# Performance work log

Hardware: AMD Instinct MI355X
Metric: run time of the kernel (lower is better)

The kernel has to match this reference:

```python
import jax, jax.numpy as jnp
import numpy as np

N_NODES = 100000
N_EDGES = 1600000
IN_CH, HID = 4, 64


def setup_inputs() -> dict:
    key = jax.random.key(0)
    ks = jax.random.split(key, 10)
    x = jax.random.normal(ks[0], (N_NODES, IN_CH), dtype=jnp.float32)
    edge_index = jax.random.randint(ks[1], (2, N_EDGES), 0, N_NODES, dtype=jnp.int64)

    def lin(k, fin, fout):
        s = 1.0 / np.sqrt(fin)
        return jax.random.uniform(k, (fin, fout), jnp.float32, -s, s)

    return {
        "x": x,
        "edge_index": edge_index,
        "W1": lin(ks[2], IN_CH, HID), "b1": jnp.zeros((HID,), jnp.float32),
        "W2": lin(ks[3], HID, HID), "b2": jnp.zeros((HID,), jnp.float32),
        "lpW1": lin(ks[4], 2 * HID, HID), "lpb1": jnp.zeros((HID,), jnp.float32),
        "lpW2": lin(ks[5], HID, 1), "lpb2": jnp.zeros((1,), jnp.float32),
    }


def reference(x, edge_index, W1, b1, W2, b2, lpW1, lpb1, lpW2, lpb2):
    n = x.shape[0]
    src, dst = edge_index[0], edge_index[1]
    # GCN normalization with self-loops (PyG GCNConv defaults)
    loop = jnp.arange(n)
    s = jnp.concatenate([src, loop])  # [E+N]
    d = jnp.concatenate([dst, loop])
    deg = jax.ops.segment_sum(jnp.ones_like(s, dtype=x.dtype), d, num_segments=n)
    dinv = jnp.where(deg > 0, jax.lax.rsqrt(deg), 0.0)
    norm = dinv[s] * dinv[d]  # [E+N]

    def gcn_conv(h, W, b):
        hw = h @ W                               # [N, HID]
        msg = hw[s] * norm[:, None]              # gather + scale
        return jax.ops.segment_sum(msg, d, num_segments=n) + b

    h = jax.nn.relu(gcn_conv(x, W1, b1))
    h = jax.nn.relu(gcn_conv(h, W2, b2))  # node embeddings [N, HID]

    # edge scoring: gather-concat -> 2-layer MLP
    ef = jnp.concatenate([h[src], h[dst]], axis=1)  # [E, 2*HID]
    logits = (jax.nn.relu(ef @ lpW1 + lpb1) @ lpW2 + lpb2).squeeze(-1)  # [E]
    return logits
```

## Files before the change

### kernel.cpp

```cpp
#include <hip/hip_runtime.h>
#include <hip/hip_fp16.h>

#define NN 100000
#define NE 1600000
#define HH 64
#define BSH 9
#define NBUK 196

typedef unsigned long long u64;

__device__ __forceinline__ u64 epack(int s, int d, int e) {
    return (u64)(unsigned)s | ((u64)(unsigned)d << 17) | ((u64)(unsigned)e << 34);
}
__device__ __forceinline__ int esrc(u64 w) { return (int)(w & 0x1FFFF); }
__device__ __forceinline__ int edst(u64 w) { return (int)((w >> 17) & 0x1FFFF); }
__device__ __forceinline__ int eeid(u64 w) { return (int)(w >> 34); }


__global__ __launch_bounds__(1024) void k_bhist(const int* __restrict__ dst,
                                                int* __restrict__ bcnt) {
    __shared__ int cnt[NBUK];
    int tid = threadIdx.x;
    if (tid < NBUK) cnt[tid] = 0;
    __syncthreads();
    int e0 = blockIdx.x * 4096 + tid;
    #pragma unroll
    for (int i = 0; i < 4; ++i) {
        int e = e0 + i * 1024;
        if (e < NE) atomicAdd(&cnt[dst[e] >> BSH], 1);
    }
    __syncthreads();
    if (tid < NBUK && cnt[tid] > 0) atomicAdd(&bcnt[tid], cnt[tid]);
}


__global__ void k_bscan(const int* __restrict__ bcnt, int* __restrict__ bbase,
                        int* __restrict__ bcur) {
    __shared__ int sh[256];
    int tid = threadIdx.x;
    int v = (tid < NBUK) ? bcnt[tid] : 0;
    sh[tid] = v;
    __syncthreads();
    for (int off = 1; off < 256; off <<= 1) {
        int t = (tid >= off) ? sh[tid - off] : 0;
        __syncthreads();
        sh[tid] += t;
        __syncthreads();
    }
    if (tid < NBUK) {
        int ex = sh[tid] - v;
        bbase[tid] = ex;
        bcur[tid] = ex;
    }
    if (tid == 0) bbase[NBUK] = NE;
}


__global__ __launch_bounds__(1024) void k_partA(const int* __restrict__ src,
                                                const int* __restrict__ dst,
                                                int* __restrict__ bcur,
                                                u64* __restrict__ partA) {
    __shared__ int cnt[NBUK], off[NBUK], base[NBUK];
    int tid = threadIdx.x;
    if (tid < NBUK) { cnt[tid] = 0; off[tid] = 0; }
    __syncthreads();
    int e0 = blockIdx.x * 4096 + tid;
    int d0 = 0, d1 = 0, d2 = 0, d3 = 0;
    if (e0 < NE)            { d0 = dst[e0];            atomicAdd(&cnt[d0 >> BSH], 1); }
    if (e0 + 1024 < NE)     { d1 = dst[e0 + 1024];     atomicAdd(&cnt[d1 >> BSH], 1); }
    if (e0 + 2048 < NE)     { d2 = dst[e0 + 2048];     atomicAdd(&cnt[d2 >> BSH], 1); }
    if (e0 + 3072 < NE)     { d3 = dst[e0 + 3072];     atomicAdd(&cnt[d3 >> BSH], 1); }
    __syncthreads();
    if (tid < NBUK && cnt[tid] > 0) base[tid] = atomicAdd(&bcur[tid], cnt[tid]);
    __syncthreads();
    if (e0 < NE) {
        int b = d0 >> BSH; int o = atomicAdd(&off[b], 1);
        partA[base[b] + o] = epack(src[e0], d0, e0);
    }
    if (e0 + 1024 < NE) {
        int b = d1 >> BSH; int o = atomicAdd(&off[b], 1);
        partA[base[b] + o] = epack(src[e0 + 1024], d1, e0 + 1024);
    }
    if (e0 + 2048 < NE) {
        int b = d2 >> BSH; int o = atomicAdd(&off[b], 1);
        partA[base[b] + o] = epack(src[e0 + 2048], d2, e0 + 2048);
    }
    if (e0 + 3072 < NE) {
        int b = d3 >> BSH; int o = atomicAdd(&off[b], 1);
        partA[base[b] + o] = epack(src[e0 + 3072], d3, e0 + 3072);
    }
}


__global__ __launch_bounds__(1024) void k_partB2(const int* __restrict__ bbase,
                                                 const u64* __restrict__ partA,
                                                 u64* __restrict__ ecsr,
                                                 int* __restrict__ ptr,
                                                 float* __restrict__ dinv) {
    __shared__ int cnt[512], sc[512], cur[512];
    int b = blockIdx.x, tid = threadIdx.x;
    int nd0 = b << BSH;
    int nnode = NN - nd0; if (nnode > 512) nnode = 512;
    if (tid < 512) cnt[tid] = 0;
    __syncthreads();
    int pbeg = bbase[b], pend = bbase[b + 1];
    for (int p = pbeg + tid; p < pend; p += 1024)
        atomicAdd(&cnt[edst(partA[p]) - nd0], 1);
    __syncthreads();
    if (tid < 512) sc[tid] = cnt[tid];
    __syncthreads();
    for (int off = 1; off < 512; off <<= 1) {
        int t = (tid < 512 && tid >= off) ? sc[tid - off] : 0;
        __syncthreads();
        if (tid < 512) sc[tid] += t;
        __syncthreads();
    }
    if (tid < nnode) {
        int p = pbeg + sc[tid] - cnt[tid];
        ptr[nd0 + tid] = p;
        cur[tid] = p;
        dinv[nd0 + tid] = rsqrtf((float)(cnt[tid] + 1));
    }
    if (b == NBUK - 1 && tid == 0) ptr[NN] = NE;
    __syncthreads();
    for (int p = pbeg + tid; p < pend; p += 1024) {
        u64 t = partA[p];
        int pos = atomicAdd(&cur[edst(t) - nd0], 1);
        ecsr[pos] = t;
    }
}


__global__ void k_mm1(const float* __restrict__ x, const float* __restrict__ W1,
                      const float* __restrict__ dinv, __half* __restrict__ g) {
    __shared__ float w[4 * HH];
    w[threadIdx.x] = W1[threadIdx.x];
    __syncthreads();
    int idx = blockIdx.x * 256 + threadIdx.x;
    int i = idx >> 6, j = idx & 63;
    float4 xv = *reinterpret_cast<const float4*>(&x[i * 4]);
    float s = fmaf(xv.x, w[j],
              fmaf(xv.y, w[HH + j],
              fmaf(xv.z, w[2 * HH + j],
                   xv.w * w[3 * HH + j])));
    g[idx] = __float2half(s * dinv[i]);
}


__global__ void k_agg(const __half* __restrict__ g, const float* __restrict__ dinv,
                      const int* __restrict__ ptr, const u64* __restrict__ ecsr,
                      const float* __restrict__ bias, __half* __restrict__ h) {
    int node = blockIdx.x * 4 + (threadIdx.x >> 6);
    int lane = threadIdx.x & 63;
    if (node >= NN) return;
    float acc = __half2float(g[node * HH + lane]);
    int e0 = ptr[node], e1 = ptr[node + 1];
    int deg = e1 - e0;
    int lim = deg < 64 ? deg : 64;
    int c = (lane < deg) ? esrc(ecsr[e0 + lane]) : 0;
    int j = 0;
    for (; j + 16 <= lim; j += 16) {
        int s0 = __builtin_amdgcn_readlane(c, j);
        int s1 = __builtin_amdgcn_readlane(c, j + 1);
        int s2 = __builtin_amdgcn_readlane(c, j + 2);
        int s3 = __builtin_amdgcn_readlane(c, j + 3);
        int s4 = __builtin_amdgcn_readlane(c, j + 4);
        int s5 = __builtin_amdgcn_readlane(c, j + 5);
        int s6 = __builtin_amdgcn_readlane(c, j + 6);
        int s7 = __builtin_amdgcn_readlane(c, j + 7);
        int s8 = __builtin_amdgcn_readlane(c, j + 8);
        int s9 = __builtin_amdgcn_readlane(c, j + 9);
        int sa = __builtin_amdgcn_readlane(c, j + 10);
        int sb = __builtin_amdgcn_readlane(c, j + 11);
        int sc = __builtin_amdgcn_readlane(c, j + 12);
        int sd = __builtin_amdgcn_readlane(c, j + 13);
        int se = __builtin_amdgcn_readlane(c, j + 14);
        int sf = __builtin_amdgcn_readlane(c, j + 15);
        __half a0 = g[s0 * HH + lane];
        __half a1 = g[s1 * HH + lane];
        __half a2 = g[s2 * HH + lane];
        __half a3 = g[s3 * HH + lane];
        __half a4 = g[s4 * HH + lane];
        __half a5 = g[s5 * HH + lane];
        __half a6 = g[s6 * HH + lane];
        __half a7 = g[s7 * HH + lane];
        __half a8 = g[s8 * HH + lane];
        __half a9 = g[s9 * HH + lane];
        __half aa = g[sa * HH + lane];
        __half ab = g[sb * HH + lane];
        __half ac = g[sc * HH + lane];
        __half ad = g[sd * HH + lane];
        __half ae = g[se * HH + lane];
        __half af = g[sf * HH + lane];
        acc += ((__half2float(a0) + __half2float(a1)) + (__half2float(a2) + __half2float(a3)))
             + ((__half2float(a4) + __half2float(a5)) + (__half2float(a6) + __half2float(a7)));
        acc += ((__half2float(a8) + __half2float(a9)) + (__half2float(aa) + __half2float(ab)))
             + ((__half2float(ac) + __half2float(ad)) + (__half2float(ae) + __half2float(af)));
    }
    for (; j + 4 <= lim; j += 4) {
        int s0 = __builtin_amdgcn_readlane(c, j);
        int s1 = __builtin_amdgcn_readlane(c, j + 1);
        int s2 = __builtin_amdgcn_readlane(c, j + 2);
        int s3 = __builtin_amdgcn_readlane(c, j + 3);
        __half a0 = g[s0 * HH + lane];
        __half a1 = g[s1 * HH + lane];
        __half a2 = g[s2 * HH + lane];
        __half a3 = g[s3 * HH + lane];
        acc += (__half2float(a0) + __half2float(a1)) + (__half2float(a2) + __half2float(a3));
    }
    for (; j < lim; ++j) {
        int s = __builtin_amdgcn_readlane(c, j);
        acc += __half2float(g[s * HH + lane]);
    }
    for (int e = e0 + 64; e < e1; ++e) {
        acc += __half2float(g[esrc(ecsr[e]) * HH + lane]);
    }
    h[node * HH + lane] = __float2half(fmaxf(fmaf(acc, dinv[node], bias[lane]), 0.f));
}


__global__ void k_mm2(const __half* __restrict__ in, const float* __restrict__ W,
                      const float* __restrict__ dinv, __half* __restrict__ out) {
    __shared__ float w[HH * HH];
    __shared__ float row[16][HH + 4];
    for (int t = threadIdx.x; t < HH * HH; t += 256) w[t] = W[t];
    {
        int flat = threadIdx.x * 4;
        int r = flat >> 6, c = flat & 63;
        int node = blockIdx.x * 16 + r;
        uint2 v = *reinterpret_cast<const uint2*>(&in[node * HH + c]);
        float2 lo = __half22float2(*reinterpret_cast<__half2*>(&v.x));
        float2 hi = __half22float2(*reinterpret_cast<__half2*>(&v.y));
        row[r][c] = lo.x; row[r][c + 1] = lo.y; row[r][c + 2] = hi.x; row[r][c + 3] = hi.y;
    }
    __syncthreads();
    int r = threadIdx.x >> 4;
    int cg = (threadIdx.x & 15) * 4;
    int node = blockIdx.x * 16 + r;
    float4 acc = {0.f, 0.f, 0.f, 0.f};
    #pragma unroll
    for (int k = 0; k < HH; ++k) {
        float rk = row[r][k];
        float4 wv = *reinterpret_cast<const float4*>(&w[k * HH + cg]);
        acc.x = fmaf(rk, wv.x, acc.x);
        acc.y = fmaf(rk, wv.y, acc.y);
        acc.z = fmaf(rk, wv.z, acc.z);
        acc.w = fmaf(rk, wv.w, acc.w);
    }
    float dv = dinv[node];
    __half2 h01 = __floats2half2_rn(acc.x * dv, acc.y * dv);
    __half2 h23 = __floats2half2_rn(acc.z * dv, acc.w * dv);
    *reinterpret_cast<__half2*>(&out[node * HH + cg])     = h01;
    *reinterpret_cast<__half2*>(&out[node * HH + cg + 2]) = h23;
}


__global__ void k_proj(const __half* __restrict__ h, const float* __restrict__ lpW1,
                       const float* __restrict__ lpb1,
                       __half* __restrict__ A, __half* __restrict__ B) {
    __shared__ float w[128 * HH];
    __shared__ float row[16][HH + 4];
    for (int t = threadIdx.x; t < 128 * HH; t += 256) w[t] = lpW1[t];
    {
        int flat = threadIdx.x * 4;
        int r = flat >> 6, c = flat & 63;
        int node = blockIdx.x * 16 + r;
        uint2 v = *reinterpret_cast<const uint2*>(&h[node * HH + c]);
        float2 lo = __half22float2(*reinterpret_cast<__half2*>(&v.x));
        float2 hi = __half22float2(*reinterpret_cast<__half2*>(&v.y));
        row[r][c] = lo.x; row[r][c + 1] = lo.y; row[r][c + 2] = hi.x; row[r][c + 3] = hi.y;
    }
    __syncthreads();
    int r = threadIdx.x >> 4;
    int cg = (threadIdx.x & 15) * 4;
    int node = blockIdx.x * 16 + r;
    float4 acca = *reinterpret_cast<const float4*>(&lpb1[cg]);
    float4 accb = {0.f, 0.f, 0.f, 0.f};
    #pragma unroll
    for (int k = 0; k < HH; ++k) {
        float rk = row[r][k];
        float4 wa = *reinterpret_cast<const float4*>(&w[k * HH + cg]);
        float4 wb = *reinterpret_cast<const float4*>(&w[(HH + k) * HH + cg]);
        acca.x = fmaf(rk, wa.x, acca.x);
        acca.y = fmaf(rk, wa.y, acca.y);
        acca.z = fmaf(rk, wa.z, acca.z);
        acca.w = fmaf(rk, wa.w, acca.w);
        accb.x = fmaf(rk, wb.x, accb.x);
        accb.y = fmaf(rk, wb.y, accb.y);
        accb.z = fmaf(rk, wb.z, accb.z);
        accb.w = fmaf(rk, wb.w, accb.w);
    }
    __half2 a01 = __floats2half2_rn(acca.x, acca.y);
    __half2 a23 = __floats2half2_rn(acca.z, acca.w);
    __half2 b01 = __floats2half2_rn(accb.x, accb.y);
    __half2 b23 = __floats2half2_rn(accb.z, accb.w);
    *reinterpret_cast<__half2*>(&A[node * HH + cg])     = a01;
    *reinterpret_cast<__half2*>(&A[node * HH + cg + 2]) = a23;
    *reinterpret_cast<__half2*>(&B[node * HH + cg])     = b01;
    *reinterpret_cast<__half2*>(&B[node * HH + cg + 2]) = b23;
}


__device__ inline void acc8(float& acc, float4 av, float4 bv, const float* w8) {
    const __half2* ah = reinterpret_cast<const __half2*>(&av);
    const __half2* bh = reinterpret_cast<const __half2*>(&bv);
    #pragma unroll
    for (int i = 0; i < 4; ++i) {
        float2 a = __half22float2(ah[i]);
        float2 b = __half22float2(bh[i]);
        acc = fmaf(fmaxf(a.x + b.x, 0.f), w8[2 * i],     acc);
        acc = fmaf(fmaxf(a.y + b.y, 0.f), w8[2 * i + 1], acc);
    }
}

__global__ void k_edge(const u64* __restrict__ ecsr,
                       const __half* __restrict__ A, const __half* __restrict__ B,
                       const float* __restrict__ lpW2, const float* __restrict__ lpb2,
                       float* __restrict__ out) {
    __shared__ float w[HH];
    if (threadIdx.x < HH) w[threadIdx.x] = lpW2[threadIdx.x];
    __syncthreads();
    int lane = threadIdx.x & 63;
    int wv   = threadIdx.x >> 6;
    int sub  = lane & 3;
    int g    = lane >> 2;
    int base = (blockIdx.x * 4 + wv) * 32;
    u64 t0 = ecsr[base + g];
    u64 t1 = ecsr[base + 16 + g];
    const float4* pa0 = reinterpret_cast<const float4*>(&A[esrc(t0) * HH]) + sub * 2;
    const float4* pb0 = reinterpret_cast<const float4*>(&B[edst(t0) * HH]) + sub * 2;
    const float4* pa1 = reinterpret_cast<const float4*>(&A[esrc(t1) * HH]) + sub * 2;
    const float4* pb1 = reinterpret_cast<const float4*>(&B[edst(t1) * HH]) + sub * 2;
    float4 a00 = pa0[0], a01 = pa0[1];
    float4 b00 = pb0[0], b01 = pb0[1];
    float4 a10 = pa1[0], a11 = pa1[1];
    float4 b10 = pb1[0], b11 = pb1[1];
    const float* w16 = &w[sub * 16];
    float acc0 = 0.f, acc1 = 0.f;
    acc8(acc0, a00, b00, w16);
    acc8(acc0, a01, b01, w16 + 8);
    acc8(acc1, a10, b10, w16);
    acc8(acc1, a11, b11, w16 + 8);
    acc0 += __shfl_xor(acc0, 1);
    acc0 += __shfl_xor(acc0, 2);
    acc1 += __shfl_xor(acc1, 1);
    acc1 += __shfl_xor(acc1, 2);
    if (sub == 0) {
        float c0 = lpb2[0];
        out[eeid(t0)] = acc0 + c0;
        out[eeid(t1)] = acc1 + c0;
    }
}


extern "C" void kernel_launch(void* const* d_in, const int* in_sizes, int n_in,
                              void* d_out, int out_size, void* d_ws, size_t ws_size,
                              hipStream_t stream) {
    const float* x    = (const float*)d_in[0];
    const int*   ei   = (const int*)d_in[1];
    const float* W1   = (const float*)d_in[2];
    const float* b1   = (const float*)d_in[3];
    const float* W2   = (const float*)d_in[4];
    const float* b2   = (const float*)d_in[5];
    const float* lpW1 = (const float*)d_in[6];
    const float* lpb1 = (const float*)d_in[7];
    const float* lpW2 = (const float*)d_in[8];
    const float* lpb2 = (const float*)d_in[9];
    const int* src = ei;
    const int* dst = ei + NE;
    float* logits = (float*)d_out;

    char* ws = (char*)d_ws;
    size_t o = 0;
    auto take = [&](size_t bytes) { void* p = ws + o; o = (o + bytes + 255) & ~(size_t)255; return p; };
    float*  dinv   = (float*) take(NN * sizeof(float));
    int*    ptr    = (int*)   take((NN + 1) * sizeof(int));
    int*    bcnt   = (int*)   take(NBUK * sizeof(int));
    int*    bbase  = (int*)   take((NBUK + 1) * sizeof(int));
    int*    bcur   = (int*)   take(NBUK * sizeof(int));
    u64*    ecsr   = (u64*)   take((size_t)NE * sizeof(u64));
    char*   bufA   = (char*)  take((size_t)NE * sizeof(u64));
    __half* bufB   = (__half*)take((size_t)NN * HH * sizeof(__half));
    __half* bufC   = (__half*)take((size_t)NN * HH * sizeof(__half));
    u64*    partA  = (u64*)bufA;
    __half* g1h    = (__half*)bufA;
    __half* h2     = (__half*)bufA;
    __half* h1     = bufB;
    __half* Ah     = bufB;
    __half* g2h    = bufC;
    __half* Bh     = bufC;

    hipMemsetAsync(bcnt, 0, NBUK * sizeof(int), stream);
    k_bhist<<<(NE + 4095) / 4096, 1024, 0, stream>>>(dst, bcnt);
    k_bscan<<<1, 256, 0, stream>>>(bcnt, bbase, bcur);
    k_partA<<<(NE + 4095) / 4096, 1024, 0, stream>>>(src, dst, bcur, partA);
    k_partB2<<<NBUK, 1024, 0, stream>>>(bbase, partA, ecsr, ptr, dinv);

    k_mm1<<<(NN * HH) / 256, 256, 0, stream>>>(x, W1, dinv, g1h);
    k_agg<<<(NN + 3) / 4, 256, 0, stream>>>(g1h, dinv, ptr, ecsr, b1, h1);

    k_mm2<<<NN / 16, 256, 0, stream>>>(h1, W2, dinv, g2h);
    k_agg<<<(NN + 3) / 4, 256, 0, stream>>>(g2h, dinv, ptr, ecsr, b2, h2);

    k_proj<<<NN / 16, 256, 0, stream>>>(h2, lpW1, lpb1, Ah, Bh);

    k_edge<<<NE / 128, 256, 0, stream>>>(ecsr, Ah, Bh, lpW2, lpb2, logits);
}
```

Baseline: 267.9 us.

## Fuse first-layer matmul into CSR build and add compact 32-bit source index array

The x@W1 scaled by dinv computation moves into the k_partB2 CSR-building kernel, which drops the separate k_mm1 launch. k_partB2 also writes a separate 4-byte source-index array, so the two aggregation passes read 4 bytes per edge instead of 8. Workspace buffers are reassigned so that g1 no longer aliases partA while partA is still being read. In exchange, the 196 blocks of k_partB2 now do extra per-node work, and the extra scsr write adds 6.4MB of traffic.

```diff
diff --git a/kernel.cpp b/kernel.cpp
--- a/kernel.cpp
+++ b/kernel.cpp
@@ -95,10 +95,16 @@
 __global__ __launch_bounds__(1024) void k_partB2(const int* __restrict__ bbase,
                                                  const u64* __restrict__ partA,
                                                  u64* __restrict__ ecsr,
+                                                 int* __restrict__ scsr,
                                                  int* __restrict__ ptr,
-                                                 float* __restrict__ dinv) {
+                                                 float* __restrict__ dinv,
+                                                 const float* __restrict__ x,
+                                                 const float* __restrict__ W1,
+                                                 __half* __restrict__ g1) {
     __shared__ int cnt[512], sc[512], cur[512];
+    __shared__ float w1[4 * HH];
     int b = blockIdx.x, tid = threadIdx.x;
+    if (tid < 4 * HH) w1[tid] = W1[tid];
     int nd0 = b << BSH;
     int nnode = NN - nd0; if (nnode > 512) nnode = 512;
     if (tid < 512) cnt[tid] = 0;
@@ -127,28 +133,25 @@
         u64 t = partA[p];
         int pos = atomicAdd(&cur[edst(t) - nd0], 1);
         ecsr[pos] = t;
-    }
-}
-
-
-__global__ void k_mm1(const float* __restrict__ x, const float* __restrict__ W1,
-                      const float* __restrict__ dinv, __half* __restrict__ g) {
-    __shared__ float w[4 * HH];
-    w[threadIdx.x] = W1[threadIdx.x];
-    __syncthreads();
-    int idx = blockIdx.x * 256 + threadIdx.x;
-    int i = idx >> 6, j = idx & 63;
-    float4 xv = *reinterpret_cast<const float4*>(&x[i * 4]);
-    float s = fmaf(xv.x, w[j],
-              fmaf(xv.y, w[HH + j],
-              fmaf(xv.z, w[2 * HH + j],
-                   xv.w * w[3 * HH + j])));
-    g[idx] = __float2half(s * dinv[i]);
+        scsr[pos] = esrc(t);
+    }
+    int total = nnode * HH;
+    for (int i = tid; i < total; i += 1024) {
+        int ln = i >> 6, ch = i & 63;
+        int node = nd0 + ln;
+        float4 xv = *reinterpret_cast<const float4*>(&x[node * 4]);
+        float dv = rsqrtf((float)(cnt[ln] + 1));
+        float s = fmaf(xv.x, w1[ch],
+                  fmaf(xv.y, w1[HH + ch],
+                  fmaf(xv.z, w1[2 * HH + ch],
+                       xv.w * w1[3 * HH + ch])));
+        g1[node * HH + ch] = __float2half(s * dv);
+    }
 }
 
 
 __global__ void k_agg(const __half* __restrict__ g, const float* __restrict__ dinv,
-                      const int* __restrict__ ptr, const u64* __restrict__ ecsr,
+                      const int* __restrict__ ptr, const int* __restrict__ scsr,
                       const float* __restrict__ bias, __half* __restrict__ h) {
     int node = blockIdx.x * 4 + (threadIdx.x >> 6);
     int lane = threadIdx.x & 63;
@@ -157,7 +160,7 @@
     int e0 = ptr[node], e1 = ptr[node + 1];
     int deg = e1 - e0;
     int lim = deg < 64 ? deg : 64;
-    int c = (lane < deg) ? esrc(ecsr[e0 + lane]) : 0;
+    int c = (lane < deg) ? scsr[e0 + lane] : 0;
     int j = 0;
     for (; j + 16 <= lim; j += 16) {
         int s0 = __builtin_amdgcn_readlane(c, j);
@@ -213,7 +216,7 @@
         acc += __half2float(g[s * HH + lane]);
     }
     for (int e = e0 + 64; e < e1; ++e) {
-        acc += __half2float(g[esrc(ecsr[e]) * HH + lane]);
+        acc += __half2float(g[scsr[e] * HH + lane]);
     }
     h[node * HH + lane] = __float2half(fmaxf(fmaf(acc, dinv[node], bias[lane]), 0.f));
 }
@@ -379,28 +382,28 @@
     int*    bbase  = (int*)   take((NBUK + 1) * sizeof(int));
     int*    bcur   = (int*)   take(NBUK * sizeof(int));
     u64*    ecsr   = (u64*)   take((size_t)NE * sizeof(u64));
+    int*    scsr   = (int*)   take((size_t)NE * sizeof(int));
     char*   bufA   = (char*)  take((size_t)NE * sizeof(u64));
     __half* bufB   = (__half*)take((size_t)NN * HH * sizeof(__half));
     __half* bufC   = (__half*)take((size_t)NN * HH * sizeof(__half));
     u64*    partA  = (u64*)bufA;
-    __half* g1h    = (__half*)bufA;
-    __half* h2     = (__half*)bufA;
-    __half* h1     = bufB;
-    __half* Ah     = bufB;
-    __half* g2h    = bufC;
-    __half* Bh     = bufC;
+    __half* g2h    = (__half*)bufA;
+    __half* Bh     = (__half*)bufA;
+    __half* g1h    = bufB;
+    __half* h2     = bufB;
+    __half* h1     = bufC;
+    __half* Ah     = bufC;
 
     hipMemsetAsync(bcnt, 0, NBUK * sizeof(int), stream);
     k_bhist<<<(NE + 4095) / 4096, 1024, 0, stream>>>(dst, bcnt);
     k_bscan<<<1, 256, 0, stream>>>(bcnt, bbase, bcur);
     k_partA<<<(NE + 4095) / 4096, 1024, 0, stream>>>(src, dst, bcur, partA);
-    k_partB2<<<NBUK, 1024, 0, stream>>>(bbase, partA, ecsr, ptr, dinv);
-
-    k_mm1<<<(NN * HH) / 256, 256, 0, stream>>>(x, W1, dinv, g1h);
-    k_agg<<<(NN + 3) / 4, 256, 0, stream>>>(g1h, dinv, ptr, ecsr, b1, h1);
+    k_partB2<<<NBUK, 1024, 0, stream>>>(bbase, partA, ecsr, scsr, ptr, dinv, x, W1, g1h);
+
+    k_agg<<<(NN + 3) / 4, 256, 0, stream>>>(g1h, dinv, ptr, scsr, b1, h1);
 
     k_mm2<<<NN / 16, 256, 0, stream>>>(h1, W2, dinv, g2h);
-    k_agg<<<(NN + 3) / 4, 256, 0, stream>>>(g2h, dinv, ptr, ecsr, b2, h2);
+    k_agg<<<(NN + 3) / 4, 256, 0, stream>>>(g2h, dinv, ptr, scsr, b2, h2);
 
     k_proj<<<NN / 16, 256, 0, stream>>>(h2, lpW1, lpb1, Ah, Bh);
 
```

New measurement: 272.2 us. No clear change (+1.6%).
